# Kernel optimization log

Hardware: AMD Instinct MI355X
Metric: run time of the kernel (lower is better)

## Reference

```python
import jax, jax.numpy as jnp
import numpy as np

N, E, F, H, C, T = 100000, 1600000, 128, 64, 8, 4

def setup_inputs() -> dict:
    key = jax.random.key(0)
    ks = jax.random.split(key, 16)
    inp = {
        'x': jax.random.normal(ks[0], (N, F), dtype=jnp.float32),
        'node_types': jax.random.randint(ks[1], (N,), 0, T, dtype=jnp.int64),
        'edge_index0': jax.random.randint(ks[2], (2, E), 0, N, dtype=jnp.int64),
        'edge_index1': jax.random.randint(ks[3], (2, E), 0, N, dtype=jnp.int64),
        # per-node-type input projections
        'W_in': jax.random.normal(ks[4], (T, F, H), dtype=jnp.float32) / np.sqrt(F),
        'b_in': jnp.zeros((T, H), dtype=jnp.float32),
        # 4 GCN convs (layer0: paths [0,0],[0,1]; layer1: paths [0,0],[1,0])
        'W_conv': jax.random.normal(ks[5], (4, H, H), dtype=jnp.float32) / np.sqrt(H),
        'b_conv': jnp.zeros((4, H), dtype=jnp.float32),
        # output attention/classifier layers
        'W1': jax.random.normal(ks[6], (H, H), dtype=jnp.float32) / np.sqrt(H),
        'b1': jnp.zeros((H,), dtype=jnp.float32),
        'W2': jax.random.normal(ks[7], (H, 1), dtype=jnp.float32) / np.sqrt(H),
        'b2': jnp.zeros((1,), dtype=jnp.float32),
        'W3': jax.random.normal(ks[8], (H, C), dtype=jnp.float32) / np.sqrt(H),
        'b3': jnp.zeros((C,), dtype=jnp.float32),
    }
    return inp


def gcn_conv(x, edge_index, W, b):
    # PyG GCNConv: add self-loops, symmetric normalization, then scatter-add.
    n = x.shape[0]
    loop = jnp.arange(n, dtype=edge_index.dtype)
    src = jnp.concatenate([edge_index[0], loop])
    dst = jnp.concatenate([edge_index[1], loop])
    deg = jax.ops.segment_sum(jnp.ones_like(dst, dtype=x.dtype), dst, num_segments=n)
    dinv = jnp.where(deg > 0, jax.lax.rsqrt(deg), 0.0)
    norm = dinv[src] * dinv[dst]            # [E+N]
    xw = x @ W                              # [N,H]
    msg = xw[src] * norm[:, None]           # [E+N,H]
    out = jax.ops.segment_sum(msg, dst, num_segments=n)
    return out + b


def reference(x, node_types, edge_index0, edge_index1,
              W_in, b_in, W_conv, b_conv, W1, b1, W2, b2, W3, b3):
    # per-node-type input linear (fixed small loop over T types)
    hid = jnp.zeros((x.shape[0], H), dtype=x.dtype)
    for t in range(T):
        ht = x @ W_in[t] + b_in[t]
        hid = jnp.where((node_types == t)[:, None], ht, hid)
    edges = [edge_index0, edge_index1]
    states = [hid]
    # layer 0: paths [state 0, adj 0], [state 0, adj 1]; layer_agg = max
    h0 = gcn_conv(states[0], edges[0], W_conv[0], b_conv[0])
    h1 = gcn_conv(states[0], edges[1], W_conv[1], b_conv[1])
    states.append(jnp.maximum(h0, h1))
    # layer 1: paths [state 0, adj 0], [state 1, adj 0]
    h2 = gcn_conv(states[0], edges[0], W_conv[2], b_conv[2])
    h3 = gcn_conv(states[1], edges[0], W_conv[3], b_conv[3])
    states.append(jnp.maximum(h2, h3))
    # LayerNorm (no affine) + gelu (torch default = exact erf form)
    tmp = states[-1]
    mu = jnp.mean(tmp, axis=-1, keepdims=True)
    var = jnp.mean(jnp.square(tmp - mu), axis=-1, keepdims=True)
    tmp = (tmp - mu) * jax.lax.rsqrt(var + 1e-5)
    hidi = jax.nn.gelu(tmp, approximate=False)
    # attention combine over (single) temp state
    attn = jax.nn.softmax(jnp.tanh(hidi @ W1 + b1) @ W2 + b2, axis=-1)  # [N,1] -> ones
    out = attn * hidi
    return out @ W3 + b3
```

## Files before the change

### kernel.cpp

```cpp
#include <hip/hip_runtime.h>
#include <hip/hip_bf16.h>
#include <math.h>


#define HID   64
#define RB    128
#define CHUNK 4096

__device__ __forceinline__ float bf2f(ushort v) {
    unsigned u = ((unsigned)v) << 16;
    return __int_as_float((int)u);
}
__device__ __forceinline__ ushort f2bf(float f) {
    unsigned u = __float_as_uint(f);
    unsigned r = u + 0x7FFFu + ((u >> 16) & 1u);
    return (ushort)(r >> 16);
}
__device__ __forceinline__ void addbf(float a[4], uint2 v) {
    a[0] += __int_as_float((int)(v.x << 16));
    a[1] += __int_as_float((int)(v.x & 0xFFFF0000u));
    a[2] += __int_as_float((int)(v.y << 16));
    a[3] += __int_as_float((int)(v.y & 0xFFFF0000u));
}

__global__ void histA(const int* __restrict__ dst0, const int* __restrict__ dst1,
                      int E, unsigned M, int* __restrict__ bcnt) {
    __shared__ int h[2 * RB];
    for (int i = threadIdx.x; i < 2 * RB; i += blockDim.x) h[i] = 0;
    __syncthreads();
    int stride = gridDim.x * blockDim.x;
    for (int i = blockIdx.x * blockDim.x + threadIdx.x; i < E; i += stride) {
        atomicAdd(&h[__umulhi((unsigned)dst0[i], M)], 1);
        atomicAdd(&h[RB + __umulhi((unsigned)dst1[i], M)], 1);
    }
    __syncthreads();
    for (int i = threadIdx.x; i < 2 * RB; i += blockDim.x)
        if (h[i]) atomicAdd(&bcnt[i], h[i]);
}

__global__ void scanA(const int* __restrict__ bcnt, int* __restrict__ bbase,
                      int* __restrict__ bcur, int E,
                      int* __restrict__ off0, int* __restrict__ off1, int N) {
    __shared__ int t[2 * RB];
    int tid = threadIdx.x;
    int orig = bcnt[tid];
    t[tid] = orig;
    __syncthreads();
    int list = tid >> 7, r = tid & (RB - 1);
    for (int o = 1; o < RB; o <<= 1) {
        int u = (r >= o) ? t[tid - o] : 0;
        __syncthreads();
        t[tid] += u;
        __syncthreads();
    }
    int incl = t[tid];
    int excl = incl - orig;
    bbase[list * (RB + 1) + r] = excl;
    bcur[tid] = excl;
    if (r == RB - 1) bbase[list * (RB + 1) + RB] = incl;
    if (tid == 0) { off0[N] = E; off1[N] = E; }
}

__global__ void __launch_bounds__(256) partB(const int* __restrict__ e0,
                                             const int* __restrict__ e1,
                                             int E, int BW, unsigned M,
                                             int* __restrict__ bcur_all,
                                             unsigned* __restrict__ arena_all) {
    __shared__ int hist[RB], scn[RB], lbase[RB], cur[RB], gbase[RB];
    __shared__ uint2 buf[CHUNK];
    int half = gridDim.x >> 1;
    int list = (blockIdx.x >= half) ? 1 : 0;
    const int* src = list ? e1 : e0;
    const int* dst = src + E;
    int* bcur = bcur_all + list * RB;
    unsigned* arena = arena_all + (size_t)list * E;
    int blk = blockIdx.x - list * half;
    int tid = threadIdx.x;

    for (int c0 = blk * CHUNK; c0 < E; c0 += half * CHUNK) {
        int cn = min(CHUNK, E - c0);
        for (int i = tid; i < RB; i += 256) hist[i] = 0;
        __syncthreads();
        unsigned ls[16], ld[16];
        #pragma unroll
        for (int k = 0; k < 16; ++k) {
            int j = k * 256 + tid;
            ld[k] = 0xFFFFFFFFu; ls[k] = 0;
            if (j < cn) {
                ls[k] = (unsigned)src[c0 + j];
                ld[k] = (unsigned)dst[c0 + j];
                atomicAdd(&hist[__umulhi(ld[k], M)], 1);
            }
        }
        __syncthreads();
        if (tid < RB) scn[tid] = hist[tid];
        __syncthreads();
        for (int o = 1; o < RB; o <<= 1) {
            int u = (tid < RB && tid >= o) ? scn[tid - o] : 0;
            __syncthreads();
            if (tid < RB) scn[tid] += u;
            __syncthreads();
        }
        if (tid < RB) {
            int ex = scn[tid] - hist[tid];
            lbase[tid] = ex;
            cur[tid]   = ex;
            gbase[tid] = hist[tid] ? atomicAdd(&bcur[tid], hist[tid]) : 0;
        }
        __syncthreads();
        #pragma unroll
        for (int k = 0; k < 16; ++k) {
            if (ld[k] != 0xFFFFFFFFu) {
                int b = __umulhi(ld[k], M);
                int slot = atomicAdd(&cur[b], 1);
                buf[slot] = make_uint2(ls[k], ld[k]);
            }
        }
        __syncthreads();
        for (int i = tid; i < cn; i += 256) {
            uint2 p = buf[i];
            int b = __umulhi(p.y, M);
            arena[gbase[b] + (i - lbase[b])] = (p.x << 10) | (p.y - (unsigned)(b * BW));
        }
        __syncthreads();
    }
}

__global__ void __launch_bounds__(1024) buildC(const unsigned* __restrict__ arena_all,
                                               const int* __restrict__ bbase,
                                               int E, int N, int BW,
                                               int* __restrict__ csr0, int* __restrict__ csr1,
                                               int* __restrict__ off0, int* __restrict__ off1,
                                               float* __restrict__ dinv0, float* __restrict__ dinv1) {
    __shared__ int degl[800], scn[800], cur[800];
    int list = blockIdx.x >> 7, rb = blockIdx.x & (RB - 1);
    const unsigned* arena = arena_all + (size_t)list * E;
    int* csr = list ? csr1 : csr0;
    int* off = list ? off1 : off0;
    float* dinv = list ? dinv1 : dinv0;
    int base = bbase[list * (RB + 1) + rb];
    int end  = bbase[list * (RB + 1) + rb + 1];
    int nbase = rb * BW;
    int nn = min(BW, N - nbase);
    if (nn <= 0) return;
    int tid = threadIdx.x;
    for (int i = tid; i < nn; i += 1024) degl[i] = 0;
    __syncthreads();
    for (int j = base + tid; j < end; j += 1024)
        atomicAdd(&degl[arena[j] & 1023u], 1);
    __syncthreads();
    int v0 = (tid < nn) ? degl[tid] : 0;
    if (tid < nn) scn[tid] = v0;
    __syncthreads();
    for (int o = 1; o < nn; o <<= 1) {
        int u = (tid < nn && tid >= o) ? scn[tid - o] : 0;
        __syncthreads();
        if (tid < nn) scn[tid] += u;
        __syncthreads();
    }
    if (tid < nn) {
        int ex = scn[tid] - v0;
        cur[tid] = ex;
        off[nbase + tid] = base + ex;
        dinv[nbase + tid] = rsqrtf((float)(v0 + 1));
    }
    __syncthreads();
    for (int j = base + tid; j < end; j += 1024) {
        unsigned p = arena[j];
        int loc = atomicAdd(&cur[p & 1023u], 1);
        csr[base + loc] = (int)(p >> 10);
    }
}

__global__ void input_proj(const float* __restrict__ x, const int* __restrict__ types,
                           const float* __restrict__ W_in, const float* __restrict__ b_in,
                           const float* __restrict__ dinv0, const float* __restrict__ dinv1,
                           ushort* __restrict__ g0, ushort* __restrict__ g1,
                           int N, int F) {
    __shared__ float xs[4 * 128];
    int tid = threadIdx.x;
    int w = tid >> 6, h = tid & 63;
    int n0 = blockIdx.x * 4;
    for (int i = tid; i < 4 * F; i += 256) {
        int nn = n0 + i / F;
        xs[i] = (nn < N) ? x[(size_t)nn * F + (i % F)] : 0.0f;
    }
    __syncthreads();
    int n = n0 + w;
    if (n >= N) return;
    int t = types[n];
    const float* W = W_in + (size_t)t * F * HID;
    float acc = b_in[t * HID + h];
    const float* xr = xs + w * F;
    #pragma unroll 4
    for (int f = 0; f < F; ++f)
        acc = fmaf(xr[f], W[(size_t)f * HID + h], acc);
    size_t idx = (size_t)n * HID + h;
    g0[idx] = f2bf(acc * dinv0[n]);
    g1[idx] = f2bf(acc * dinv1[n]);
}

__global__ void layer1(const ushort* __restrict__ g0, const ushort* __restrict__ g1,
                       const int* __restrict__ off0, const int* __restrict__ csr0,
                       const float* __restrict__ dinv0,
                       const int* __restrict__ off1, const int* __restrict__ csr1,
                       const float* __restrict__ dinv1,
                       const float* __restrict__ W_conv, const float* __restrict__ b_conv,
                       float* __restrict__ t0, ushort* __restrict__ s1g, int N) {
    __shared__ float l0[4][HID], l1[4][HID];
    int w = threadIdx.x >> 6, lane = threadIdx.x & 63;
    int n = blockIdx.x * 4 + w;
    if (n >= N) return;
    int q = lane >> 4, fl = lane & 15;
    const uint2* G0 = (const uint2*)g0;
    const uint2* G1 = (const uint2*)g1;
    float a0[4] = {0, 0, 0, 0}, a1[4] = {0, 0, 0, 0};
    if (q == 0) {
        addbf(a0, G0[(size_t)n * 16 + fl]);
        addbf(a1, G1[(size_t)n * 16 + fl]);
    }
    {
        int e = off0[n], e_ = off0[n + 1];
        for (; e + 8 <= e_; e += 8) {
            int ia = csr0[e + q], ib = csr0[e + 4 + q];
            uint2 va = G0[(size_t)ia * 16 + fl];
            uint2 vb = G0[(size_t)ib * 16 + fl];
            addbf(a0, va); addbf(a0, vb);
        }
        if (e + 4 <= e_) {
            int ia = csr0[e + q];
            addbf(a0, G0[(size_t)ia * 16 + fl]);
            e += 4;
        }
        int rem = e_ - e;
        if (rem > 0) {
            int ia = csr0[e + (q < rem ? q : rem - 1)];
            uint2 va = G0[(size_t)ia * 16 + fl];
            if (q < rem) addbf(a0, va);
        }
    }
    {
        int e = off1[n], e_ = off1[n + 1];
        for (; e + 8 <= e_; e += 8) {
            int ia = csr1[e + q], ib = csr1[e + 4 + q];
            uint2 va = G1[(size_t)ia * 16 + fl];
            uint2 vb = G1[(size_t)ib * 16 + fl];
            addbf(a1, va); addbf(a1, vb);
        }
        if (e + 4 <= e_) {
            int ia = csr1[e + q];
            addbf(a1, G1[(size_t)ia * 16 + fl]);
            e += 4;
        }
        int rem = e_ - e;
        if (rem > 0) {
            int ia = csr1[e + (q < rem ? q : rem - 1)];
            uint2 va = G1[(size_t)ia * 16 + fl];
            if (q < rem) addbf(a1, va);
        }
    }
    float d0 = dinv0[n], d1 = dinv1[n];
    #pragma unroll
    for (int k = 0; k < 4; ++k) {
        a0[k] += __shfl_xor(a0[k], 16, 64);
        a0[k] += __shfl_xor(a0[k], 32, 64);
        a1[k] += __shfl_xor(a1[k], 16, 64);
        a1[k] += __shfl_xor(a1[k], 32, 64);
        a0[k] *= d0;
        a1[k] *= d1;
    }
    if (q == 0) {
        *(float4*)&l0[w][fl * 4] = make_float4(a0[0], a0[1], a0[2], a0[3]);
        *(float4*)&l1[w][fl * 4] = make_float4(a1[0], a1[1], a1[2], a1[3]);
        *(float4*)&t0[(size_t)n * HID + fl * 4] = make_float4(a0[0], a0[1], a0[2], a0[3]);
    }
    int h = lane;
    const float* W0 = W_conv;
    const float* W1 = W_conv + HID * HID;
    float m0 = b_conv[h];
    float m1 = b_conv[HID + h];
    #pragma unroll 8
    for (int k = 0; k < HID; ++k) {
        m0 = fmaf(l0[w][k], W0[k * HID + h], m0);
        m1 = fmaf(l1[w][k], W1[k * HID + h], m1);
    }
    s1g[(size_t)n * HID + h] = f2bf(fmaxf(m0, m1) * d0);
}

__global__ void layer2(const float* __restrict__ t0, const ushort* __restrict__ s1g,
                       const int* __restrict__ off0, const int* __restrict__ csr0,
                       const float* __restrict__ dinv0,
                       const float* __restrict__ W_conv, const float* __restrict__ b_conv,
                       const float* __restrict__ W3, const float* __restrict__ b3,
                       float* __restrict__ out, int N) {
    __shared__ float l2[4][HID], l3[4][HID], gs[4][HID];
    int w = threadIdx.x >> 6, lane = threadIdx.x & 63;
    int n = blockIdx.x * 4 + w;
    if (n >= N) return;
    int q = lane >> 4, fl = lane & 15;
    const uint2* S = (const uint2*)s1g;
    float a[4] = {0, 0, 0, 0};
    if (q == 0) addbf(a, S[(size_t)n * 16 + fl]);
    {
        int e = off0[n], e_ = off0[n + 1];
        for (; e + 8 <= e_; e += 8) {
            int ia = csr0[e + q], ib = csr0[e + 4 + q];
            uint2 va = S[(size_t)ia * 16 + fl];
            uint2 vb = S[(size_t)ib * 16 + fl];
            addbf(a, va); addbf(a, vb);
        }
        if (e + 4 <= e_) {
            int ia = csr0[e + q];
            addbf(a, S[(size_t)ia * 16 + fl]);
            e += 4;
        }
        int rem = e_ - e;
        if (rem > 0) {
            int ia = csr0[e + (q < rem ? q : rem - 1)];
            uint2 va = S[(size_t)ia * 16 + fl];
            if (q < rem) addbf(a, va);
        }
    }
    float d0 = dinv0[n];
    #pragma unroll
    for (int k = 0; k < 4; ++k) {
        a[k] += __shfl_xor(a[k], 16, 64);
        a[k] += __shfl_xor(a[k], 32, 64);
        a[k] *= d0;
    }
    if (q == 0)
        *(float4*)&l3[w][fl * 4] = make_float4(a[0], a[1], a[2], a[3]);
    int h = lane;
    l2[w][h] = t0[(size_t)n * HID + h];
    const float* W2  = W_conv + 2 * HID * HID;
    const float* W3c = W_conv + 3 * HID * HID;
    float m2 = b_conv[2 * HID + h];
    float m3 = b_conv[3 * HID + h];
    #pragma unroll 8
    for (int k = 0; k < HID; ++k) {
        m2 = fmaf(l2[w][k], W2[k * HID + h], m2);
        m3 = fmaf(l3[w][k], W3c[k * HID + h], m3);
    }
    float s2 = fmaxf(m2, m3);
    float sum = s2;
    #pragma unroll
    for (int off = 32; off; off >>= 1) sum += __shfl_xor(sum, off, 64);
    float mu = sum * (1.0f / 64.0f);
    float dv = s2 - mu;
    float v = dv * dv;
    #pragma unroll
    for (int off = 32; off; off >>= 1) v += __shfl_xor(v, off, 64);
    float xn = dv * rsqrtf(v * (1.0f / 64.0f) + 1e-5f);
    float g = 0.5f * xn * (1.0f + erff(xn * 0.70710678118654752f));
    gs[w][h] = g;
    if (h < 8) {
        float acc = b3[h];
        #pragma unroll 8
        for (int k = 0; k < HID; ++k)
            acc = fmaf(gs[w][k], W3[k * 8 + h], acc);
        out[(size_t)n * 8 + h] = acc;
    }
}

extern "C" void kernel_launch(void* const* d_in, const int* in_sizes, int n_in,
                              void* d_out, int out_size, void* d_ws, size_t ws_size,
                              hipStream_t stream) {
    const float* x          = (const float*)d_in[0];
    const int*   node_types = (const int*)d_in[1];
    const int*   e0         = (const int*)d_in[2];
    const int*   e1         = (const int*)d_in[3];
    const float* W_in       = (const float*)d_in[4];
    const float* b_in       = (const float*)d_in[5];
    const float* W_conv     = (const float*)d_in[6];
    const float* b_conv     = (const float*)d_in[7];
    const float* W3         = (const float*)d_in[12];
    const float* b3         = (const float*)d_in[13];
    float* out = (float*)d_out;

    int N = in_sizes[1];
    int F = in_sizes[0] / N;
    int E = in_sizes[2] / 2;
    int BW = (N + RB - 1) / RB;
    unsigned M = (unsigned)(0x100000000ULL / (unsigned long long)BW) + 1u;

    int*   bcnt  = (int*)d_ws;
    int*   bbase = bcnt + 2 * RB;
    int*   bcur  = bbase + 2 * (RB + 1);
    int*   off0  = bcur + 2 * RB + 6;
    int*   off1  = off0 + (N + 1);
    float* dinv0 = (float*)(off1 + (N + 1));
    float* dinv1 = dinv0 + N;
    int*   csr0  = (int*)(dinv1 + N);
    int*   csr1  = csr0 + E;
    ushort* g0   = (ushort*)(csr1 + E);
    ushort* g1   = g0 + (size_t)HID * N;
    float* t0    = (float*)(g1 + (size_t)HID * N);
    ushort* s1g  = (ushort*)(t0 + (size_t)HID * N);
    unsigned* arena = (unsigned*)t0;

    (void)hipMemsetAsync(bcnt, 0, 2 * RB * sizeof(int), stream);
    histA<<<1024, 256, 0, stream>>>(e0 + E, e1 + E, E, M, bcnt);
    scanA<<<1, 256, 0, stream>>>(bcnt, bbase, bcur, E, off0, off1, N);
    partB<<<256, 256, 0, stream>>>(e0, e1, E, BW, M, bcur, arena);
    buildC<<<2 * RB, 1024, 0, stream>>>(arena, bbase, E, N, BW,
                                        csr0, csr1, off0, off1, dinv0, dinv1);
    input_proj<<<(N + 3) / 4, 256, 0, stream>>>(x, node_types, W_in, b_in,
                                                dinv0, dinv1, g0, g1, N, F);
    layer1<<<(N + 3) / 4, 256, 0, stream>>>(g0, g1, off0, csr0, dinv0, off1, csr1, dinv1,
                                            W_conv, b_conv, t0, s1g, N);
    layer2<<<(N + 3) / 4, 256, 0, stream>>>(t0, s1g, off0, csr0, dinv0,
                                            W_conv, b_conv, W3, b3, out, N);
}
```

Measured before the change: 543.3 us.

## Pad CSR rows to multiples of eight with sentinel node and packed offsets

Builds padded CSR rows (degree rounded up to 8, filled with a sentinel node index N whose feature row and dinv are zero) and packs base offset plus iteration count into one word, so the gather loops have no tail handling. Stores a single unnormalized bf16 projection instead of two dinv-scaled copies and applies source dinv per edge during the gather. Also stores the layer-0 intermediate as bf16, caches conv weights as bf16 in shared memory, and uses 512-thread blocks. This cuts memory traffic and branching, but pads edges, adds per-edge dinv loads, and costs some precision.

```diff
diff --git a/kernel.cpp b/kernel.cpp
--- a/kernel.cpp
+++ b/kernel.cpp
@@ -7,20 +7,20 @@
 #define RB    128
 #define CHUNK 4096
 
-__device__ __forceinline__ float bf2f(ushort v) {
-    unsigned u = ((unsigned)v) << 16;
-    return __int_as_float((int)u);
-}
+__device__ __forceinline__ float bflo(unsigned u) { return __int_as_float((int)(u << 16)); }
+__device__ __forceinline__ float bfhi(unsigned u) { return __int_as_float((int)(u & 0xFFFF0000u)); }
+__device__ __forceinline__ float bf2f(ushort v) { return __int_as_float((int)(((unsigned)v) << 16)); }
 __device__ __forceinline__ ushort f2bf(float f) {
     unsigned u = __float_as_uint(f);
     unsigned r = u + 0x7FFFu + ((u >> 16) & 1u);
     return (ushort)(r >> 16);
 }
-__device__ __forceinline__ void addbf(float a[4], uint2 v) {
-    a[0] += __int_as_float((int)(v.x << 16));
-    a[1] += __int_as_float((int)(v.x & 0xFFFF0000u));
-    a[2] += __int_as_float((int)(v.y << 16));
-    a[3] += __int_as_float((int)(v.y & 0xFFFF0000u));
+
+__global__ void zeroRow(unsigned* __restrict__ ghz, unsigned* __restrict__ s1z,
+                        float* __restrict__ dinv0, float* __restrict__ dinv1, int N) {
+    int tid = threadIdx.x;
+    if (tid < 32) { ghz[tid] = 0u; s1z[tid] = 0u; }
+    if (tid == 0) { dinv0[N] = 0.0f; dinv1[N] = 0.0f; }
 }
 
 __global__ void histA(const int* __restrict__ dst0, const int* __restrict__ dst1,
@@ -39,8 +39,7 @@
 }
 
 __global__ void scanA(const int* __restrict__ bcnt, int* __restrict__ bbase,
-                      int* __restrict__ bcur, int E,
-                      int* __restrict__ off0, int* __restrict__ off1, int N) {
+                      int* __restrict__ bcur) {
     __shared__ int t[2 * RB];
     int tid = threadIdx.x;
     int orig = bcnt[tid];
@@ -58,7 +57,6 @@
     bbase[list * (RB + 1) + r] = excl;
     bcur[tid] = excl;
     if (r == RB - 1) bbase[list * (RB + 1) + RB] = incl;
-    if (tid == 0) { off0[N] = E; off1[N] = E; }
 }
 
 __global__ void __launch_bounds__(256) partB(const int* __restrict__ e0,
@@ -129,17 +127,18 @@
 __global__ void __launch_bounds__(1024) buildC(const unsigned* __restrict__ arena_all,
                                                const int* __restrict__ bbase,
                                                int E, int N, int BW,
-                                               int* __restrict__ csr0, int* __restrict__ csr1,
-                                               int* __restrict__ off0, int* __restrict__ off1,
+                                               int* __restrict__ csr0p, int* __restrict__ csr1p,
+                                               unsigned* __restrict__ offp0, unsigned* __restrict__ offp1,
                                                float* __restrict__ dinv0, float* __restrict__ dinv1) {
     __shared__ int degl[800], scn[800], cur[800];
     int list = blockIdx.x >> 7, rb = blockIdx.x & (RB - 1);
     const unsigned* arena = arena_all + (size_t)list * E;
-    int* csr = list ? csr1 : csr0;
-    int* off = list ? off1 : off0;
+    int* csr = list ? csr1p : csr0p;
+    unsigned* offp = list ? offp1 : offp0;
     float* dinv = list ? dinv1 : dinv0;
     int base = bbase[list * (RB + 1) + rb];
     int end  = bbase[list * (RB + 1) + rb + 1];
+    int csrb = base + 8 * BW * rb;
     int nbase = rb * BW;
     int nn = min(BW, N - nbase);
     if (nn <= 0) return;
@@ -149,8 +148,9 @@
     for (int j = base + tid; j < end; j += 1024)
         atomicAdd(&degl[arena[j] & 1023u], 1);
     __syncthreads();
-    int v0 = (tid < nn) ? degl[tid] : 0;
-    if (tid < nn) scn[tid] = v0;
+    int d = (tid < nn) ? degl[tid] : 0;
+    int dp = d ? ((d + 7) & ~7) : 0;
+    if (tid < nn) scn[tid] = dp;
     __syncthreads();
     for (int o = 1; o < nn; o <<= 1) {
         int u = (tid < nn && tid >= o) ? scn[tid - o] : 0;
@@ -159,24 +159,23 @@
         __syncthreads();
     }
     if (tid < nn) {
-        int ex = scn[tid] - v0;
+        int ex = scn[tid] - dp;
         cur[tid] = ex;
-        off[nbase + tid] = base + ex;
-        dinv[nbase + tid] = rsqrtf((float)(v0 + 1));
+        offp[nbase + tid] = (unsigned)(csrb + ex) | ((unsigned)(dp >> 3) << 25);
+        dinv[nbase + tid] = rsqrtf((float)(d + 1));
+        for (int j = ex + d; j < ex + dp; ++j) csr[csrb + j] = N;
     }
     __syncthreads();
     for (int j = base + tid; j < end; j += 1024) {
         unsigned p = arena[j];
         int loc = atomicAdd(&cur[p & 1023u], 1);
-        csr[base + loc] = (int)(p >> 10);
+        csr[csrb + loc] = (int)(p >> 10);
     }
 }
 
 __global__ void input_proj(const float* __restrict__ x, const int* __restrict__ types,
                            const float* __restrict__ W_in, const float* __restrict__ b_in,
-                           const float* __restrict__ dinv0, const float* __restrict__ dinv1,
-                           ushort* __restrict__ g0, ushort* __restrict__ g1,
-                           int N, int F) {
+                           ushort* __restrict__ gh, int N, int F) {
     __shared__ float xs[4 * 128];
     int tid = threadIdx.x;
     int w = tid >> 6, h = tid & 63;
@@ -195,71 +194,90 @@
     #pragma unroll 4
     for (int f = 0; f < F; ++f)
         acc = fmaf(xr[f], W[(size_t)f * HID + h], acc);
-    size_t idx = (size_t)n * HID + h;
-    g0[idx] = f2bf(acc * dinv0[n]);
-    g1[idx] = f2bf(acc * dinv1[n]);
-}
-
-__global__ void layer1(const ushort* __restrict__ g0, const ushort* __restrict__ g1,
-                       const int* __restrict__ off0, const int* __restrict__ csr0,
-                       const float* __restrict__ dinv0,
-                       const int* __restrict__ off1, const int* __restrict__ csr1,
-                       const float* __restrict__ dinv1,
-                       const float* __restrict__ W_conv, const float* __restrict__ b_conv,
-                       float* __restrict__ t0, ushort* __restrict__ s1g, int N) {
-    __shared__ float l0[4][HID], l1[4][HID];
-    int w = threadIdx.x >> 6, lane = threadIdx.x & 63;
-    int n = blockIdx.x * 4 + w;
+    gh[(size_t)n * HID + h] = f2bf(acc);
+}
+
+__device__ __forceinline__ void gather_w(const uint2* __restrict__ GH,
+                                         const float* __restrict__ dv,
+                                         const int* __restrict__ csr,
+                                         unsigned wword, int q, int fl, float a[4]) {
+    int base = (int)(wword & 0x1FFFFFFu);
+    int it = (int)(wword >> 25);
+    if (it == 0) return;
+    const int* cp = csr + base;
+    int ia = cp[q], ib = cp[4 + q];
+    while (true) {
+        uint2 va = GH[(size_t)ia * 16 + fl];
+        uint2 vb = GH[(size_t)ib * 16 + fl];
+        float wa = dv[ia], wb = dv[ib];
+        --it; cp += 8;
+        int na = 0, nb = 0;
+        if (it > 0) { na = cp[q]; nb = cp[4 + q]; }
+        a[0] = fmaf(bflo(va.x), wa, a[0]);
+        a[1] = fmaf(bfhi(va.x), wa, a[1]);
+        a[2] = fmaf(bflo(va.y), wa, a[2]);
+        a[3] = fmaf(bfhi(va.y), wa, a[3]);
+        a[0] = fmaf(bflo(vb.x), wb, a[0]);
+        a[1] = fmaf(bfhi(vb.x), wb, a[1]);
+        a[2] = fmaf(bflo(vb.y), wb, a[2]);
+        a[3] = fmaf(bfhi(vb.y), wb, a[3]);
+        if (it == 0) break;
+        ia = na; ib = nb;
+    }
+}
+
+__device__ __forceinline__ void gather_u(const uint2* __restrict__ GH,
+                                         const int* __restrict__ csr,
+                                         unsigned wword, int q, int fl, float a[4]) {
+    int base = (int)(wword & 0x1FFFFFFu);
+    int it = (int)(wword >> 25);
+    if (it == 0) return;
+    const int* cp = csr + base;
+    int ia = cp[q], ib = cp[4 + q];
+    while (true) {
+        uint2 va = GH[(size_t)ia * 16 + fl];
+        uint2 vb = GH[(size_t)ib * 16 + fl];
+        --it; cp += 8;
+        int na = 0, nb = 0;
+        if (it > 0) { na = cp[q]; nb = cp[4 + q]; }
+        a[0] += bflo(va.x) + bflo(vb.x);
+        a[1] += bfhi(va.x) + bfhi(vb.x);
+        a[2] += bflo(va.y) + bflo(vb.y);
+        a[3] += bfhi(va.y) + bfhi(vb.y);
+        if (it == 0) break;
+        ia = na; ib = nb;
+    }
+}
+
+__global__ void __launch_bounds__(512) gatherL1(
+        const ushort* __restrict__ gh,
+        const unsigned* __restrict__ offp0, const int* __restrict__ csr0p,
+        const float* __restrict__ dinv0,
+        const unsigned* __restrict__ offp1, const int* __restrict__ csr1p,
+        const float* __restrict__ dinv1,
+        const float* __restrict__ W_conv, const float* __restrict__ b_conv,
+        unsigned* __restrict__ a0g, ushort* __restrict__ s1g, int N) {
+    __shared__ ushort Wb[2 * HID * HID];
+    __shared__ float l0[8][HID], l1[8][HID];
+    int tid = threadIdx.x;
+    for (int i = tid; i < 2 * HID * HID; i += 512) Wb[i] = f2bf(W_conv[i]);
+    __syncthreads();
+    int w = tid >> 6, lane = tid & 63;
+    int q = lane >> 4, fl = lane & 15;
+    int n = blockIdx.x * 8 + w;
     if (n >= N) return;
-    int q = lane >> 4, fl = lane & 15;
-    const uint2* G0 = (const uint2*)g0;
-    const uint2* G1 = (const uint2*)g1;
+    const uint2* GH = (const uint2*)gh;
+    float d0 = dinv0[n], d1 = dinv1[n];
     float a0[4] = {0, 0, 0, 0}, a1[4] = {0, 0, 0, 0};
     if (q == 0) {
-        addbf(a0, G0[(size_t)n * 16 + fl]);
-        addbf(a1, G1[(size_t)n * 16 + fl]);
-    }
-    {
-        int e = off0[n], e_ = off0[n + 1];
-        for (; e + 8 <= e_; e += 8) {
-            int ia = csr0[e + q], ib = csr0[e + 4 + q];
-            uint2 va = G0[(size_t)ia * 16 + fl];
-            uint2 vb = G0[(size_t)ib * 16 + fl];
-            addbf(a0, va); addbf(a0, vb);
-        }
-        if (e + 4 <= e_) {
-            int ia = csr0[e + q];
-            addbf(a0, G0[(size_t)ia * 16 + fl]);
-            e += 4;
-        }
-        int rem = e_ - e;
-        if (rem > 0) {
-            int ia = csr0[e + (q < rem ? q : rem - 1)];
-            uint2 va = G0[(size_t)ia * 16 + fl];
-            if (q < rem) addbf(a0, va);
-        }
-    }
-    {
-        int e = off1[n], e_ = off1[n + 1];
-        for (; e + 8 <= e_; e += 8) {
-            int ia = csr1[e + q], ib = csr1[e + 4 + q];
-            uint2 va = G1[(size_t)ia * 16 + fl];
-            uint2 vb = G1[(size_t)ib * 16 + fl];
-            addbf(a1, va); addbf(a1, vb);
-        }
-        if (e + 4 <= e_) {
-            int ia = csr1[e + q];
-            addbf(a1, G1[(size_t)ia * 16 + fl]);
-            e += 4;
-        }
-        int rem = e_ - e;
-        if (rem > 0) {
-            int ia = csr1[e + (q < rem ? q : rem - 1)];
-            uint2 va = G1[(size_t)ia * 16 + fl];
-            if (q < rem) addbf(a1, va);
-        }
-    }
-    float d0 = dinv0[n], d1 = dinv1[n];
+        uint2 sv = GH[(size_t)n * 16 + fl];
+        a0[0] = bflo(sv.x) * d0; a0[1] = bfhi(sv.x) * d0;
+        a0[2] = bflo(sv.y) * d0; a0[3] = bfhi(sv.y) * d0;
+        a1[0] = bflo(sv.x) * d1; a1[1] = bfhi(sv.x) * d1;
+        a1[2] = bflo(sv.y) * d1; a1[3] = bfhi(sv.y) * d1;
+    }
+    gather_w(GH, dinv0, csr0p, offp0[n], q, fl, a0);
+    gather_w(GH, dinv1, csr1p, offp1[n], q, fl, a1);
     #pragma unroll
     for (int k = 0; k < 4; ++k) {
         a0[k] += __shfl_xor(a0[k], 16, 64);
@@ -272,56 +290,51 @@
     if (q == 0) {
         *(float4*)&l0[w][fl * 4] = make_float4(a0[0], a0[1], a0[2], a0[3]);
         *(float4*)&l1[w][fl * 4] = make_float4(a1[0], a1[1], a1[2], a1[3]);
-        *(float4*)&t0[(size_t)n * HID + fl * 4] = make_float4(a0[0], a0[1], a0[2], a0[3]);
+        uint2 pk;
+        pk.x = (unsigned)f2bf(a0[0]) | ((unsigned)f2bf(a0[1]) << 16);
+        pk.y = (unsigned)f2bf(a0[2]) | ((unsigned)f2bf(a0[3]) << 16);
+        ((uint2*)a0g)[(size_t)n * 16 + fl] = pk;
     }
     int h = lane;
-    const float* W0 = W_conv;
-    const float* W1 = W_conv + HID * HID;
     float m0 = b_conv[h];
     float m1 = b_conv[HID + h];
     #pragma unroll 8
     for (int k = 0; k < HID; ++k) {
-        m0 = fmaf(l0[w][k], W0[k * HID + h], m0);
-        m1 = fmaf(l1[w][k], W1[k * HID + h], m1);
+        m0 = fmaf(l0[w][k], bf2f(Wb[k * HID + h]), m0);
+        m1 = fmaf(l1[w][k], bf2f(Wb[HID * HID + k * HID + h]), m1);
     }
     s1g[(size_t)n * HID + h] = f2bf(fmaxf(m0, m1) * d0);
 }
 
-__global__ void layer2(const float* __restrict__ t0, const ushort* __restrict__ s1g,
-                       const int* __restrict__ off0, const int* __restrict__ csr0,
-                       const float* __restrict__ dinv0,
-                       const float* __restrict__ W_conv, const float* __restrict__ b_conv,
-                       const float* __restrict__ W3, const float* __restrict__ b3,
-                       float* __restrict__ out, int N) {
-    __shared__ float l2[4][HID], l3[4][HID], gs[4][HID];
-    int w = threadIdx.x >> 6, lane = threadIdx.x & 63;
-    int n = blockIdx.x * 4 + w;
+__global__ void __launch_bounds__(512) gatherL2(
+        const unsigned* __restrict__ a0g, const ushort* __restrict__ s1g,
+        const unsigned* __restrict__ offp0, const int* __restrict__ csr0p,
+        const float* __restrict__ dinv0,
+        const float* __restrict__ W_conv, const float* __restrict__ b_conv,
+        const float* __restrict__ W3, const float* __restrict__ b3,
+        float* __restrict__ out, int N) {
+    __shared__ ushort Wb[2 * HID * HID];
+    __shared__ float W3s[HID * 8];
+    __shared__ float l2[8][HID], l3[8][HID], gs[8][HID];
+    int tid = threadIdx.x;
+    for (int i = tid; i < 2 * HID * HID; i += 512) Wb[i] = f2bf(W_conv[2 * HID * HID + i]);
+    if (tid < HID * 8) W3s[tid] = W3[tid];
+    __syncthreads();
+    int w = tid >> 6, lane = tid & 63;
+    int q = lane >> 4, fl = lane & 15;
+    int n = blockIdx.x * 8 + w;
     if (n >= N) return;
-    int q = lane >> 4, fl = lane & 15;
     const uint2* S = (const uint2*)s1g;
+    float d0 = dinv0[n];
     float a[4] = {0, 0, 0, 0};
-    if (q == 0) addbf(a, S[(size_t)n * 16 + fl]);
-    {
-        int e = off0[n], e_ = off0[n + 1];
-        for (; e + 8 <= e_; e += 8) {
-            int ia = csr0[e + q], ib = csr0[e + 4 + q];
-            uint2 va = S[(size_t)ia * 16 + fl];
-            uint2 vb = S[(size_t)ib * 16 + fl];
-            addbf(a, va); addbf(a, vb);
-        }
-        if (e + 4 <= e_) {
-            int ia = csr0[e + q];
-            addbf(a, S[(size_t)ia * 16 + fl]);
-            e += 4;
-        }
-        int rem = e_ - e;
-        if (rem > 0) {
-            int ia = csr0[e + (q < rem ? q : rem - 1)];
-            uint2 va = S[(size_t)ia * 16 + fl];
-            if (q < rem) addbf(a, va);
-        }
-    }
-    float d0 = dinv0[n];
+    if (q == 0) {
+        uint2 sv = S[(size_t)n * 16 + fl];
+        a[0] = bflo(sv.x); a[1] = bfhi(sv.x);
+        a[2] = bflo(sv.y); a[3] = bfhi(sv.y);
+        uint2 av = ((const uint2*)a0g)[(size_t)n * 16 + fl];
+        *(float4*)&l2[w][fl * 4] = make_float4(bflo(av.x), bfhi(av.x), bflo(av.y), bfhi(av.y));
+    }
+    gather_u(S, csr0p, offp0[n], q, fl, a);
     #pragma unroll
     for (int k = 0; k < 4; ++k) {
         a[k] += __shfl_xor(a[k], 16, 64);
@@ -331,15 +344,12 @@
     if (q == 0)
         *(float4*)&l3[w][fl * 4] = make_float4(a[0], a[1], a[2], a[3]);
     int h = lane;
-    l2[w][h] = t0[(size_t)n * HID + h];
-    const float* W2  = W_conv + 2 * HID * HID;
-    const float* W3c = W_conv + 3 * HID * HID;
     float m2 = b_conv[2 * HID + h];
     float m3 = b_conv[3 * HID + h];
     #pragma unroll 8
     for (int k = 0; k < HID; ++k) {
-        m2 = fmaf(l2[w][k], W2[k * HID + h], m2);
-        m3 = fmaf(l3[w][k], W3c[k * HID + h], m3);
+        m2 = fmaf(l2[w][k], bf2f(Wb[k * HID + h]), m2);
+        m3 = fmaf(l3[w][k], bf2f(Wb[HID * HID + k * HID + h]), m3);
     }
     float s2 = fmaxf(m2, m3);
     float sum = s2;
@@ -357,7 +367,7 @@
         float acc = b3[h];
         #pragma unroll 8
         for (int k = 0; k < HID; ++k)
-            acc = fmaf(gs[w][k], W3[k * 8 + h], acc);
+            acc = fmaf(gs[w][k], W3s[k * 8 + h], acc);
         out[(size_t)n * 8 + h] = acc;
     }
 }
@@ -382,32 +392,34 @@
     int E = in_sizes[2] / 2;
     int BW = (N + RB - 1) / RB;
     unsigned M = (unsigned)(0x100000000ULL / (unsigned long long)BW) + 1u;
-
-    int*   bcnt  = (int*)d_ws;
-    int*   bbase = bcnt + 2 * RB;
-    int*   bcur  = bbase + 2 * (RB + 1);
-    int*   off0  = bcur + 2 * RB + 6;
-    int*   off1  = off0 + (N + 1);
-    float* dinv0 = (float*)(off1 + (N + 1));
-    float* dinv1 = dinv0 + N;
-    int*   csr0  = (int*)(dinv1 + N);
-    int*   csr1  = csr0 + E;
-    ushort* g0   = (ushort*)(csr1 + E);
-    ushort* g1   = g0 + (size_t)HID * N;
-    float* t0    = (float*)(g1 + (size_t)HID * N);
-    ushort* s1g  = (ushort*)(t0 + (size_t)HID * N);
-    unsigned* arena = (unsigned*)t0;
+    size_t EP = (size_t)E + 8 * (size_t)BW * RB + 64;
+
+    unsigned* ws32 = (unsigned*)d_ws;
+    int*      bcnt  = (int*)ws32;
+    int*      bbase = bcnt + 2 * RB;
+    int*      bcur  = bbase + 2 * (RB + 1);
+    unsigned* offp0 = (unsigned*)(bcur + 2 * RB + 6);
+    unsigned* offp1 = offp0 + (N + 1);
+    float*    dinv0 = (float*)(offp1 + (N + 1));
+    float*    dinv1 = dinv0 + (N + 1);
+    int*      csr0p = (int*)(dinv1 + (N + 1));
+    int*      csr1p = csr0p + EP;
+    ushort*   gh    = (ushort*)(csr1p + EP);
+    ushort*   s1g   = gh + (size_t)(N + 1) * HID;
+    unsigned* a0g   = (unsigned*)(s1g + (size_t)(N + 1) * HID);
+    unsigned* arena = a0g;
 
     (void)hipMemsetAsync(bcnt, 0, 2 * RB * sizeof(int), stream);
+    zeroRow<<<1, 64, 0, stream>>>((unsigned*)(gh + (size_t)N * HID),
+                                  (unsigned*)(s1g + (size_t)N * HID), dinv0, dinv1, N);
     histA<<<1024, 256, 0, stream>>>(e0 + E, e1 + E, E, M, bcnt);
-    scanA<<<1, 256, 0, stream>>>(bcnt, bbase, bcur, E, off0, off1, N);
+    scanA<<<1, 256, 0, stream>>>(bcnt, bbase, bcur);
     partB<<<256, 256, 0, stream>>>(e0, e1, E, BW, M, bcur, arena);
     buildC<<<2 * RB, 1024, 0, stream>>>(arena, bbase, E, N, BW,
-                                        csr0, csr1, off0, off1, dinv0, dinv1);
-    input_proj<<<(N + 3) / 4, 256, 0, stream>>>(x, node_types, W_in, b_in,
-                                                dinv0, dinv1, g0, g1, N, F);
-    layer1<<<(N + 3) / 4, 256, 0, stream>>>(g0, g1, off0, csr0, dinv0, off1, csr1, dinv1,
-                                            W_conv, b_conv, t0, s1g, N);
-    layer2<<<(N + 3) / 4, 256, 0, stream>>>(t0, s1g, off0, csr0, dinv0,
-                                            W_conv, b_conv, W3, b3, out, N);
-}
+                                        csr0p, csr1p, offp0, offp1, dinv0, dinv1);
+    input_proj<<<(N + 3) / 4, 256, 0, stream>>>(x, node_types, W_in, b_in, gh, N, F);
+    gatherL1<<<(N + 7) / 8, 512, 0, stream>>>(gh, offp0, csr0p, dinv0, offp1, csr1p, dinv1,
+                                              W_conv, b_conv, a0g, s1g, N);
+    gatherL2<<<(N + 7) / 8, 512, 0, stream>>>(a0g, s1g, offp0, csr0p, dinv0,
+                                              W_conv, b_conv, W3, b3, out, N);
+}
```

Result: faster. 518.3 us (-4.6%).
